# Kernel optimization log

Hardware: AMD Instinct MI355X
Metric: run time of the kernel (lower is better)

Reference implementation:

```python
import jax, jax.numpy as jnp
import numpy as np

N_NODES = 50000
N_EDGES = 800000
IN_CH = 3
HID = 32
OUT_CH = 16
HEADS = 8
NEG_SLOPE = 0.2  # PyG GATConv default LeakyReLU slope


def setup_inputs() -> dict:
    key = jax.random.key(0)
    ks = jax.random.split(key, 12)
    x = jax.random.normal(ks[0], (N_NODES, IN_CH), dtype=jnp.float32)
    edge_index = jax.random.randint(ks[1], (2, N_EDGES), 0, N_NODES, dtype=jnp.int64)
    # Layer 1: GATConv(3 -> 32, heads=8, concat=True)
    s1 = 1.0 / np.sqrt(IN_CH)
    W1 = jax.random.uniform(ks[2], (IN_CH, HEADS * HID), jnp.float32, -s1, s1)
    att_src1 = jax.random.uniform(ks[3], (HEADS, HID), jnp.float32, -s1, s1)
    att_dst1 = jax.random.uniform(ks[4], (HEADS, HID), jnp.float32, -s1, s1)
    bias1 = jnp.zeros((HEADS * HID,), jnp.float32)
    # Layer 2: GATConv(256 -> 16, heads=1, concat=False)
    s2 = 1.0 / np.sqrt(HEADS * HID)
    W2 = jax.random.uniform(ks[5], (HEADS * HID, 1 * OUT_CH), jnp.float32, -s2, s2)
    att_src2 = jax.random.uniform(ks[6], (1, OUT_CH), jnp.float32, -s2, s2)
    att_dst2 = jax.random.uniform(ks[7], (1, OUT_CH), jnp.float32, -s2, s2)
    bias2 = jnp.zeros((OUT_CH,), jnp.float32)
    return {"x": x, "edge_index": edge_index,
            "W1": W1, "att_src1": att_src1, "att_dst1": att_dst1, "bias1": bias1,
            "W2": W2, "att_src2": att_src2, "att_dst2": att_dst2, "bias2": bias2}


def gat_conv(x, src, dst, W, att_src, att_dst, bias, heads, out_ch, concat):
    """PyG-style GATConv (eval mode: attention dropout is identity).
    src/dst already include self-loops. Returns [N, heads*out_ch] or [N, out_ch]."""
    N = x.shape[0]
    h = (x @ W).reshape(N, heads, out_ch)                      # [N,H,C]
    a_s = jnp.einsum("nhc,hc->nh", h, att_src)                 # [N,H]
    a_d = jnp.einsum("nhc,hc->nh", h, att_dst)                 # [N,H]
    e = jax.nn.leaky_relu(a_s[src] + a_d[dst], NEG_SLOPE)      # [E,H]
    # segment softmax over incoming edges of each dst node
    m = jax.ops.segment_max(e, dst, num_segments=N)            # [N,H]
    e = jnp.exp(e - m[dst])
    denom = jax.ops.segment_sum(e, dst, num_segments=N)        # [N,H]
    alpha = e / (denom[dst] + 1e-16)                           # [E,H]
    msg = h[src] * alpha[:, :, None]                           # [E,H,C]
    out = jax.ops.segment_sum(msg, dst, num_segments=N)        # [N,H,C]
    out = out.reshape(N, heads * out_ch) if concat else out.mean(axis=1)
    return out + bias


def reference(x, edge_index, W1, att_src1, att_dst1, bias1, W2, att_src2, att_dst2, bias2):
    N = x.shape[0]
    loop = jnp.arange(N, dtype=edge_index.dtype)
    src = jnp.concatenate([edge_index[0], loop])  # add self-loops (PyG default)
    dst = jnp.concatenate([edge_index[1], loop])
    h = gat_conv(x, src, dst, W1, att_src1, att_dst1, bias1, HEADS, HID, True)
    h = jax.nn.elu(h)
    out = gat_conv(h, src, dst, W2, att_src2, att_dst2, bias2, 1, OUT_CH, False)
    return out
```

## Files before the change

kernel.cpp:

```cpp
#include <hip/hip_runtime.h>
#include <math.h>

#define N_NODES 50000
#define N_EDGES 800000
#define E_TOT   850000
#define HEADS   8
#define HID     32
#define C1      256
#define OUTC    16
#define NEG     0.2f
#define NB1     ((N_NODES + 255) / 256)

__device__ __forceinline__ float lrelu(float v) { return v > 0.0f ? v : NEG * v; }

__global__ __launch_bounds__(256) void k_setup(
    const float* __restrict__ x, const int* __restrict__ ei,
    const float* __restrict__ W1,
    const float* __restrict__ att_s1, const float* __restrict__ att_d1,
    const float* __restrict__ W2,
    const float* __restrict__ att_s2, const float* __restrict__ att_d2,
    float4* __restrict__ xp, int* __restrict__ cnt, int* __restrict__ rank,
    float* __restrict__ As1, float* __restrict__ Ad1,
    float* __restrict__ As2, float* __restrict__ Ad2)
{
    int t = threadIdx.x;
    int e = blockIdx.x * 256 + t;
    if (blockIdx.x == 0) {
        if (t < 24) {
            int k = t / 8, h = t % 8;
            float as = 0.0f, ad = 0.0f;
            for (int c = 0; c < HID; c++) {
                float w = W1[k * C1 + h * HID + c];
                as = fmaf(w, att_s1[h * HID + c], as);
                ad = fmaf(w, att_d1[h * HID + c], ad);
            }
            As1[k * 8 + h] = as; Ad1[k * 8 + h] = ad;
        }
        float as2 = 0.0f, ad2 = 0.0f;
        for (int j = 0; j < OUTC; j++) {
            float w = W2[t * OUTC + j];
            as2 = fmaf(w, att_s2[j], as2);
            ad2 = fmaf(w, att_d2[j], ad2);
        }
        As2[t] = as2; Ad2[t] = ad2;
    }
    if (e < N_NODES)
        xp[e] = make_float4(x[e * 3], x[e * 3 + 1], x[e * 3 + 2], 1.0f);
    if (e < E_TOT) {
        int d = (e < N_EDGES) ? ei[N_EDGES + e] : (e - N_EDGES);
        rank[e] = atomicAdd(&cnt[d], 1);
    }
}

__global__ void k_scan1(const int* __restrict__ cnt, int* __restrict__ part,
                        int* __restrict__ bsum)
{
    __shared__ int s[256];
    int tid = threadIdx.x;
    int i = blockIdx.x * 256 + tid;
    int v = (i < N_NODES) ? cnt[i] : 0;
    s[tid] = v;
    __syncthreads();
    for (int o = 1; o < 256; o <<= 1) {
        int t = (tid >= o) ? s[tid - o] : 0;
        __syncthreads();
        s[tid] += t;
        __syncthreads();
    }
    if (i < N_NODES) part[i] = s[tid] - v;
    if (tid == 255) bsum[blockIdx.x] = s[255];
}

__global__ void k_scan2(int* __restrict__ bsum)
{
    __shared__ int s[256];
    int tid = threadIdx.x;
    int v = (tid < NB1) ? bsum[tid] : 0;
    s[tid] = v;
    __syncthreads();
    for (int o = 1; o < 256; o <<= 1) {
        int t = (tid >= o) ? s[tid - o] : 0;
        __syncthreads();
        s[tid] += t;
        __syncthreads();
    }
    if (tid < NB1) bsum[tid] = s[tid] - v;
}

__global__ void k_scan3(const int* __restrict__ part, const int* __restrict__ bsum,
                        int* __restrict__ off)
{
    int i = blockIdx.x * 256 + threadIdx.x;
    if (i < N_NODES) off[i] = part[i] + bsum[blockIdx.x];
    if (i == 0) off[N_NODES] = E_TOT;
}

__global__ void k_fill(const int* __restrict__ ei, const int* __restrict__ rank,
                       const int* __restrict__ off, int* __restrict__ csr_src)
{
    int e = blockIdx.x * blockDim.x + threadIdx.x;
    if (e >= E_TOT) return;
    int s, d;
    if (e < N_EDGES) { s = ei[e]; d = ei[N_EDGES + e]; } else { s = d = e - N_EDGES; }
    csr_src[off[d] + rank[e]] = s;
}

__global__ __launch_bounds__(256) void k_agg1(
    const int* __restrict__ off, const int* __restrict__ csr_src,
    const float4* __restrict__ xp,
    const float* __restrict__ As1, const float* __restrict__ Ad1,
    float4* __restrict__ xaccw)
{
    int tid = threadIdx.x;
    int h = tid & 7;
    int dst = blockIdx.x * 32 + (tid >> 3);
    if (dst >= N_NODES) return;
    float s0 = As1[h], s1 = As1[8 + h], s2 = As1[16 + h];
    float d0 = Ad1[h], d1 = Ad1[8 + h], d2 = Ad1[16 + h];
    float4 xd = xp[dst];
    float ad = xd.x * d0 + xd.y * d1 + xd.z * d2;
    int beg = off[dst], end = off[dst + 1];
    float a0 = 0.0f, a1 = 0.0f, a2 = 0.0f, a3 = 0.0f;
    int nfull = beg + ((end - beg) & ~7);
    for (int base = beg; base < nfull; base += 8) {
        int sm = csr_src[base + h];
        float4 xv = xp[sm];
        #pragma unroll
        for (int j = 0; j < 8; j++) {
            float vx = __shfl(xv.x, j, 8);
            float vy = __shfl(xv.y, j, 8);
            float vz = __shfl(xv.z, j, 8);
            float as = vx * s0 + vy * s1 + vz * s2;
            float p = __expf(lrelu(as + ad));
            a0 = fmaf(p, vx, a0);
            a1 = fmaf(p, vy, a1);
            a2 = fmaf(p, vz, a2);
            a3 += p;
        }
    }
    if (nfull < end) {
        int idx = nfull + h;
        int sm = (idx < end) ? csr_src[idx] : 0;
        float4 xv = xp[sm];
        int m = end - nfull;
        for (int j = 0; j < m; j++) {
            float vx = __shfl(xv.x, j, 8);
            float vy = __shfl(xv.y, j, 8);
            float vz = __shfl(xv.z, j, 8);
            float as = vx * s0 + vy * s1 + vz * s2;
            float p = __expf(lrelu(as + ad));
            a0 = fmaf(p, vx, a0);
            a1 = fmaf(p, vy, a1);
            a2 = fmaf(p, vz, a2);
            a3 += p;
        }
    }
    xaccw[dst * 8 + h] = make_float4(a0, a1, a2, a3);
}

__global__ __launch_bounds__(256) void k_fin1h2(
    const float4* __restrict__ xaccw, const float* __restrict__ W1,
    const float* __restrict__ b1, const float* __restrict__ W2,
    const float* __restrict__ As2, const float* __restrict__ Ad2,
    float* __restrict__ h2, float* __restrict__ a_s2, float* __restrict__ a_d2)
{
    __shared__ float sW1[3 * C1];
    __shared__ float sAux[3 * C1];
    __shared__ float sW2t[OUTC][260];
    __shared__ float sElu[16][260];
    int t = threadIdx.x;
    for (int i = t; i < 3 * C1; i += 256) sW1[i] = W1[i];
    sAux[t] = b1[t]; sAux[C1 + t] = As2[t]; sAux[2 * C1 + t] = Ad2[t];
    for (int i = t; i < C1 * OUTC; i += 256) {
        int k = i >> 4, j = i & 15;
        sW2t[j][k] = W2[i];
    }
    __syncthreads();
    int n = t >> 4, l = t & 15;
    int node = blockIdx.x * 16 + n;
    float as = 0.0f, ad = 0.0f;
    for (int i = 0; i < 16; i++) {
        int c = l + 16 * i;
        int h = c >> 5;
        float4 xa = xaccw[node * 8 + h];
        float z = (xa.x * sW1[c] + xa.y * sW1[C1 + c] + xa.z * sW1[2 * C1 + c])
                  / (xa.w + 1e-16f) + sAux[c];
        float e = z > 0.0f ? z : expm1f(z);
        sElu[n][c] = e;
        as = fmaf(e, sAux[C1 + c], as);
        ad = fmaf(e, sAux[2 * C1 + c], ad);
    }
    for (int o = 1; o < 16; o <<= 1) {
        as += __shfl_xor(as, o, 64);
        ad += __shfl_xor(ad, o, 64);
    }
    if (l == 0) { a_s2[node] = as; a_d2[node] = ad; }
    __syncthreads();
    const float4* e4 = (const float4*)&sElu[n][0];
    const float4* w4 = (const float4*)&sW2t[l][0];
    float acc = 0.0f;
    #pragma unroll 8
    for (int k = 0; k < 64; k++) {
        float4 a = e4[k], b = w4[k];
        acc = fmaf(a.x, b.x, fmaf(a.y, b.y, fmaf(a.z, b.z, fmaf(a.w, b.w, acc))));
    }
    h2[node * OUTC + l] = acc;
}

__global__ __launch_bounds__(256) void k_agg2(
    const int* __restrict__ off, const int* __restrict__ csr_src,
    const float* __restrict__ a_s, const float* __restrict__ a_d,
    const float* __restrict__ h2, const float* __restrict__ bias,
    float* __restrict__ out)
{
    int tid = threadIdx.x;
    int c = tid & 15;
    int dst = blockIdx.x * 16 + (tid >> 4);
    if (dst >= N_NODES) return;
    int beg = off[dst], end = off[dst + 1];
    float ad = a_d[dst];
    float acc = 0.0f, denp = 0.0f;
    int nfull = beg + ((end - beg) & ~15);
    for (int base = beg; base < nfull; base += 16) {
        int sm = csr_src[base + c];
        float p = __expf(lrelu(a_s[sm] + ad));
        denp += p;
        #pragma unroll
        for (int j = 0; j < 16; j++) {
            int s = __shfl(sm, j, 16);
            float pj = __shfl(p, j, 16);
            acc = fmaf(pj, h2[s * OUTC + c], acc);
        }
    }
    if (nfull < end) {
        int idx = nfull + c;
        int sm = 0; float p = 0.0f;
        if (idx < end) { sm = csr_src[idx]; p = __expf(lrelu(a_s[sm] + ad)); }
        denp += p;
        int m = end - nfull;
        for (int j = 0; j < m; j++) {
            int s = __shfl(sm, j, 16);
            float pj = __shfl(p, j, 16);
            acc = fmaf(pj, h2[s * OUTC + c], acc);
        }
    }
    for (int o = 1; o < 16; o <<= 1) denp += __shfl_xor(denp, o, 16);
    out[dst * OUTC + c] = acc / (denp + 1e-16f) + bias[c];
}

extern "C" void kernel_launch(void* const* d_in, const int* in_sizes, int n_in,
                              void* d_out, int out_size, void* d_ws, size_t ws_size,
                              hipStream_t stream)
{
    (void)in_sizes; (void)n_in; (void)out_size; (void)ws_size;
    const float* x    = (const float*)d_in[0];
    const int*   ei   = (const int*)d_in[1];
    const float* W1   = (const float*)d_in[2];
    const float* as1w = (const float*)d_in[3];
    const float* ad1w = (const float*)d_in[4];
    const float* b1   = (const float*)d_in[5];
    const float* W2   = (const float*)d_in[6];
    const float* as2w = (const float*)d_in[7];
    const float* ad2w = (const float*)d_in[8];
    const float* b2   = (const float*)d_in[9];
    float* out = (float*)d_out;

    const long N = N_NODES;
    char* p = (char*)d_ws;
    auto alloc = [&](size_t elems) {
        void* r = p; p += ((elems + 3) & ~(size_t)3) * 4; return r;
    };

    float4* xp      = (float4*)alloc(N * 4);
    float4* xaccw   = (float4*)alloc(N * HEADS * 4);
    int*   cnt      = (int*)alloc(N);
    int*   part     = (int*)alloc(N);
    int*   off      = (int*)alloc(N + 1);
    int*   bsum     = (int*)alloc(256);
    int*   rank     = (int*)alloc(E_TOT);
    int*   csr_src  = (int*)alloc(E_TOT);
    float* As1      = (float*)alloc(32);
    float* Ad1      = (float*)alloc(32);
    float* As2      = (float*)alloc(C1);
    float* Ad2      = (float*)alloc(C1);
    float* h2v      = (float*)alloc(N * OUTC);
    float* a_s2     = (float*)alloc(N);
    float* a_d2     = (float*)alloc(N);

    hipMemsetAsync(cnt, 0, (size_t)N * sizeof(int), stream);

    k_setup<<<(E_TOT + 255) / 256, 256, 0, stream>>>(
        x, ei, W1, as1w, ad1w, W2, as2w, ad2w,
        xp, cnt, rank, As1, Ad1, As2, Ad2);
    k_scan1<<<NB1, 256, 0, stream>>>(cnt, part, bsum);
    k_scan2<<<1, 256, 0, stream>>>(bsum);
    k_scan3<<<NB1, 256, 0, stream>>>(part, bsum, off);
    k_fill<<<(E_TOT + 255) / 256, 256, 0, stream>>>(ei, rank, off, csr_src);

    k_agg1<<<(int)((N + 31) / 32), 256, 0, stream>>>(off, csr_src, xp, As1, Ad1, xaccw);
    k_fin1h2<<<(int)(N / 16), 256, 0, stream>>>(xaccw, W1, b1, W2, As2, Ad2, h2v, a_s2, a_d2);
    k_agg2<<<(int)((N + 15) / 16), 256, 0, stream>>>(off, csr_src, a_s2, a_d2, h2v, b2, out);
}
```

Before: 196.6 us.

## Fuse scans into single-pass kernel and merge layer-1 aggregation with finalize

Replaces the three scan kernels with one kernel that uses a last-block-done counter and a spin-wait flag to propagate block prefixes. Fuses the layer-1 edge aggregation into the finalize/h2 kernel, keeping per-node accumulators in shared memory instead of writing them to a global buffer. Each block recomputes the attention projections locally rather than in the setup kernel. The aim is fewer launches and less global traffic. The risks are that the spin-wait depends on all scan blocks being co-resident, and that the fused kernel has lower occupancy.

Result: slower. 239.3 us (+21.7%).

```diff
diff --git a/kernel.cpp b/kernel.cpp
--- a/kernel.cpp
+++ b/kernel.cpp
@@ -15,121 +15,143 @@
 
 __global__ __launch_bounds__(256) void k_setup(
     const float* __restrict__ x, const int* __restrict__ ei,
+    float4* __restrict__ xp, int* __restrict__ cnt, int* __restrict__ rank)
+{
+    int e = blockIdx.x * 256 + threadIdx.x;
+    if (e < N_NODES)
+        xp[e] = make_float4(x[e * 3], x[e * 3 + 1], x[e * 3 + 2], 1.0f);
+    if (e < E_TOT) {
+        int d = (e < N_EDGES) ? ei[N_EDGES + e] : (e - N_EDGES);
+        rank[e] = atomicAdd(&cnt[d], 1);
+    }
+}
+
+__global__ __launch_bounds__(256) void k_scanAll(
+    const int* __restrict__ cnt, int* __restrict__ off,
+    int* __restrict__ bsum, int* __restrict__ bpre, int* __restrict__ syncw)
+{
+    __shared__ int s[256];
+    __shared__ int sFlag;
+    int tid = threadIdx.x, bid = blockIdx.x;
+    int i = bid * 256 + tid;
+    int v = (i < N_NODES) ? cnt[i] : 0;
+    s[tid] = v;
+    __syncthreads();
+    for (int o = 1; o < 256; o <<= 1) {
+        int t2 = (tid >= o) ? s[tid - o] : 0;
+        __syncthreads();
+        s[tid] += t2;
+        __syncthreads();
+    }
+    int excl = s[tid] - v;
+    int total = s[255];
+    __syncthreads();
+    if (tid == 0) {
+        __hip_atomic_store(&bsum[bid], total, __ATOMIC_RELEASE, __HIP_MEMORY_SCOPE_AGENT);
+        int prev = __hip_atomic_fetch_add(&syncw[0], 1, __ATOMIC_ACQ_REL, __HIP_MEMORY_SCOPE_AGENT);
+        sFlag = (prev == NB1 - 1) ? 1 : 0;
+    }
+    __syncthreads();
+    if (sFlag) {
+        int bv = (tid < NB1) ? __hip_atomic_load(&bsum[tid], __ATOMIC_ACQUIRE, __HIP_MEMORY_SCOPE_AGENT) : 0;
+        s[tid] = bv;
+        __syncthreads();
+        for (int o = 1; o < 256; o <<= 1) {
+            int t2 = (tid >= o) ? s[tid - o] : 0;
+            __syncthreads();
+            s[tid] += t2;
+            __syncthreads();
+        }
+        if (tid < NB1)
+            __hip_atomic_store(&bpre[tid], s[tid] - bv, __ATOMIC_RELEASE, __HIP_MEMORY_SCOPE_AGENT);
+        __syncthreads();
+        if (tid == 0) {
+            __threadfence();
+            __hip_atomic_store(&syncw[1], 1, __ATOMIC_RELEASE, __HIP_MEMORY_SCOPE_AGENT);
+        }
+    }
+    if (tid == 0) {
+        while (__hip_atomic_load(&syncw[1], __ATOMIC_ACQUIRE, __HIP_MEMORY_SCOPE_AGENT) == 0)
+            __builtin_amdgcn_s_sleep(16);
+        sFlag = __hip_atomic_load(&bpre[bid], __ATOMIC_ACQUIRE, __HIP_MEMORY_SCOPE_AGENT);
+    }
+    __syncthreads();
+    int base = sFlag;
+    if (i < N_NODES) off[i] = base + excl;
+    if (i == 0) off[N_NODES] = E_TOT;
+}
+
+__global__ void k_fill(const int* __restrict__ ei, const int* __restrict__ rank,
+                       const int* __restrict__ off, int* __restrict__ csr_src)
+{
+    int e = blockIdx.x * blockDim.x + threadIdx.x;
+    if (e >= E_TOT) return;
+    int s, d;
+    if (e < N_EDGES) { s = ei[e]; d = ei[N_EDGES + e]; } else { s = d = e - N_EDGES; }
+    csr_src[off[d] + rank[e]] = s;
+}
+
+__global__ __launch_bounds__(256) void k_aggfin(
+    const int* __restrict__ off, const int* __restrict__ csr_src,
+    const float4* __restrict__ xp,
     const float* __restrict__ W1,
     const float* __restrict__ att_s1, const float* __restrict__ att_d1,
-    const float* __restrict__ W2,
+    const float* __restrict__ b1, const float* __restrict__ W2,
     const float* __restrict__ att_s2, const float* __restrict__ att_d2,
-    float4* __restrict__ xp, int* __restrict__ cnt, int* __restrict__ rank,
-    float* __restrict__ As1, float* __restrict__ Ad1,
-    float* __restrict__ As2, float* __restrict__ Ad2)
-{
+    float* __restrict__ h2, float* __restrict__ a_s2, float* __restrict__ a_d2)
+{
+    __shared__ float  sW1[3 * C1];
+    __shared__ float  sAux[3 * C1];
+    __shared__ float  sW2t[OUTC][272];
+    __shared__ float  sElu[16][272];
+    __shared__ float  sAtt[48];
+    __shared__ float4 sXac[16][8];
     int t = threadIdx.x;
-    int e = blockIdx.x * 256 + t;
-    if (blockIdx.x == 0) {
-        if (t < 24) {
-            int k = t / 8, h = t % 8;
-            float as = 0.0f, ad = 0.0f;
-            for (int c = 0; c < HID; c++) {
-                float w = W1[k * C1 + h * HID + c];
-                as = fmaf(w, att_s1[h * HID + c], as);
-                ad = fmaf(w, att_d1[h * HID + c], ad);
-            }
-            As1[k * 8 + h] = as; Ad1[k * 8 + h] = ad;
-        }
+    for (int i = t; i < 3 * C1; i += 256) sW1[i] = W1[i];
+    sAux[t] = b1[t];
+    {
         float as2 = 0.0f, ad2 = 0.0f;
         for (int j = 0; j < OUTC; j++) {
             float w = W2[t * OUTC + j];
             as2 = fmaf(w, att_s2[j], as2);
             ad2 = fmaf(w, att_d2[j], ad2);
         }
-        As2[t] = as2; Ad2[t] = ad2;
-    }
-    if (e < N_NODES)
-        xp[e] = make_float4(x[e * 3], x[e * 3 + 1], x[e * 3 + 2], 1.0f);
-    if (e < E_TOT) {
-        int d = (e < N_EDGES) ? ei[N_EDGES + e] : (e - N_EDGES);
-        rank[e] = atomicAdd(&cnt[d], 1);
-    }
-}
-
-__global__ void k_scan1(const int* __restrict__ cnt, int* __restrict__ part,
-                        int* __restrict__ bsum)
-{
-    __shared__ int s[256];
-    int tid = threadIdx.x;
-    int i = blockIdx.x * 256 + tid;
-    int v = (i < N_NODES) ? cnt[i] : 0;
-    s[tid] = v;
-    __syncthreads();
-    for (int o = 1; o < 256; o <<= 1) {
-        int t = (tid >= o) ? s[tid - o] : 0;
-        __syncthreads();
-        s[tid] += t;
-        __syncthreads();
-    }
-    if (i < N_NODES) part[i] = s[tid] - v;
-    if (tid == 255) bsum[blockIdx.x] = s[255];
-}
-
-__global__ void k_scan2(int* __restrict__ bsum)
-{
-    __shared__ int s[256];
-    int tid = threadIdx.x;
-    int v = (tid < NB1) ? bsum[tid] : 0;
-    s[tid] = v;
-    __syncthreads();
-    for (int o = 1; o < 256; o <<= 1) {
-        int t = (tid >= o) ? s[tid - o] : 0;
-        __syncthreads();
-        s[tid] += t;
-        __syncthreads();
-    }
-    if (tid < NB1) bsum[tid] = s[tid] - v;
-}
-
-__global__ void k_scan3(const int* __restrict__ part, const int* __restrict__ bsum,
-                        int* __restrict__ off)
-{
-    int i = blockIdx.x * 256 + threadIdx.x;
-    if (i < N_NODES) off[i] = part[i] + bsum[blockIdx.x];
-    if (i == 0) off[N_NODES] = E_TOT;
-}
-
-__global__ void k_fill(const int* __restrict__ ei, const int* __restrict__ rank,
-                       const int* __restrict__ off, int* __restrict__ csr_src)
-{
-    int e = blockIdx.x * blockDim.x + threadIdx.x;
-    if (e >= E_TOT) return;
-    int s, d;
-    if (e < N_EDGES) { s = ei[e]; d = ei[N_EDGES + e]; } else { s = d = e - N_EDGES; }
-    csr_src[off[d] + rank[e]] = s;
-}
-
-__global__ __launch_bounds__(256) void k_agg1(
-    const int* __restrict__ off, const int* __restrict__ csr_src,
-    const float4* __restrict__ xp,
-    const float* __restrict__ As1, const float* __restrict__ Ad1,
-    float4* __restrict__ xaccw)
-{
-    int tid = threadIdx.x;
-    int h = tid & 7;
-    int dst = blockIdx.x * 32 + (tid >> 3);
-    if (dst >= N_NODES) return;
-    float s0 = As1[h], s1 = As1[8 + h], s2 = As1[16 + h];
-    float d0 = Ad1[h], d1 = Ad1[8 + h], d2 = Ad1[16 + h];
-    float4 xd = xp[dst];
+        sAux[C1 + t] = as2; sAux[2 * C1 + t] = ad2;
+    }
+    for (int i = t; i < C1 * OUTC; i += 256) {
+        int k = i >> 4, j = i & 15;
+        sW2t[j][k] = W2[i];
+    }
+    if (t < 48) {
+        int q = t & 7, k = (t >> 3) % 3;
+        bool isD = t >= 24;
+        const float* att = isD ? att_d1 : att_s1;
+        float a = 0.0f;
+        for (int c = 0; c < HID; c++)
+            a = fmaf(W1[k * C1 + q * HID + c], att[q * HID + c], a);
+        sAtt[(isD ? 24 : 0) + k * 8 + q] = a;
+    }
+    __syncthreads();
+
+    int n = t >> 4, l = t & 15;
+    int h = l & 7, sub = l >> 3;
+    int node = blockIdx.x * 16 + n;
+    float s0 = sAtt[h],      s1 = sAtt[8 + h],  s2 = sAtt[16 + h];
+    float d0 = sAtt[24 + h], d1 = sAtt[32 + h], d2 = sAtt[40 + h];
+    float4 xd = xp[node];
     float ad = xd.x * d0 + xd.y * d1 + xd.z * d2;
-    int beg = off[dst], end = off[dst + 1];
+    int beg = off[node], end = off[node + 1];
     float a0 = 0.0f, a1 = 0.0f, a2 = 0.0f, a3 = 0.0f;
-    int nfull = beg + ((end - beg) & ~7);
-    for (int base = beg; base < nfull; base += 8) {
-        int sm = csr_src[base + h];
+    int nfull = beg + ((end - beg) & ~15);
+    for (int base = beg; base < nfull; base += 16) {
+        int sm = csr_src[base + l];
         float4 xv = xp[sm];
         #pragma unroll
         for (int j = 0; j < 8; j++) {
-            float vx = __shfl(xv.x, j, 8);
-            float vy = __shfl(xv.y, j, 8);
-            float vz = __shfl(xv.z, j, 8);
+            int jj = sub * 8 + j;
+            float vx = __shfl(xv.x, jj, 16);
+            float vy = __shfl(xv.y, jj, 16);
+            float vz = __shfl(xv.z, jj, 16);
             float as = vx * s0 + vy * s1 + vz * s2;
             float p = __expf(lrelu(as + ad));
             a0 = fmaf(p, vx, a0);
@@ -138,15 +160,15 @@
             a3 += p;
         }
     }
-    if (nfull < end) {
-        int idx = nfull + h;
-        int sm = (idx < end) ? csr_src[idx] : 0;
+    int m = end - nfull;
+    if (m > 0) {
+        int sm = csr_src[(l < m) ? (nfull + l) : nfull];
         float4 xv = xp[sm];
-        int m = end - nfull;
-        for (int j = 0; j < m; j++) {
-            float vx = __shfl(xv.x, j, 8);
-            float vy = __shfl(xv.y, j, 8);
-            float vz = __shfl(xv.z, j, 8);
+        int jbeg = sub * 8, jlim = min(jbeg + 8, m);
+        for (int j = jbeg; j < jlim; j++) {
+            float vx = __shfl(xv.x, j, 16);
+            float vy = __shfl(xv.y, j, 16);
+            float vz = __shfl(xv.z, j, 16);
             float as = vx * s0 + vy * s1 + vz * s2;
             float p = __expf(lrelu(as + ad));
             a0 = fmaf(p, vx, a0);
@@ -155,47 +177,32 @@
             a3 += p;
         }
     }
-    xaccw[dst * 8 + h] = make_float4(a0, a1, a2, a3);
-}
-
-__global__ __launch_bounds__(256) void k_fin1h2(
-    const float4* __restrict__ xaccw, const float* __restrict__ W1,
-    const float* __restrict__ b1, const float* __restrict__ W2,
-    const float* __restrict__ As2, const float* __restrict__ Ad2,
-    float* __restrict__ h2, float* __restrict__ a_s2, float* __restrict__ a_d2)
-{
-    __shared__ float sW1[3 * C1];
-    __shared__ float sAux[3 * C1];
-    __shared__ float sW2t[OUTC][260];
-    __shared__ float sElu[16][260];
-    int t = threadIdx.x;
-    for (int i = t; i < 3 * C1; i += 256) sW1[i] = W1[i];
-    sAux[t] = b1[t]; sAux[C1 + t] = As2[t]; sAux[2 * C1 + t] = Ad2[t];
-    for (int i = t; i < C1 * OUTC; i += 256) {
-        int k = i >> 4, j = i & 15;
-        sW2t[j][k] = W2[i];
-    }
-    __syncthreads();
-    int n = t >> 4, l = t & 15;
-    int node = blockIdx.x * 16 + n;
-    float as = 0.0f, ad = 0.0f;
+    a0 += __shfl_xor(a0, 8, 16);
+    a1 += __shfl_xor(a1, 8, 16);
+    a2 += __shfl_xor(a2, 8, 16);
+    a3 += __shfl_xor(a3, 8, 16);
+    if (sub == 0) sXac[n][h] = make_float4(a0, a1, a2, a3);
+    __syncthreads();
+
+    float as2v = 0.0f, ad2v = 0.0f;
     for (int i = 0; i < 16; i++) {
         int c = l + 16 * i;
-        int h = c >> 5;
-        float4 xa = xaccw[node * 8 + h];
+        int hh = c >> 5;
+        float4 xa = sXac[n][hh];
         float z = (xa.x * sW1[c] + xa.y * sW1[C1 + c] + xa.z * sW1[2 * C1 + c])
                   / (xa.w + 1e-16f) + sAux[c];
         float e = z > 0.0f ? z : expm1f(z);
         sElu[n][c] = e;
-        as = fmaf(e, sAux[C1 + c], as);
-        ad = fmaf(e, sAux[2 * C1 + c], ad);
+        as2v = fmaf(e, sAux[C1 + c], as2v);
+        ad2v = fmaf(e, sAux[2 * C1 + c], ad2v);
     }
     for (int o = 1; o < 16; o <<= 1) {
-        as += __shfl_xor(as, o, 64);
-        ad += __shfl_xor(ad, o, 64);
-    }
-    if (l == 0) { a_s2[node] = as; a_d2[node] = ad; }
-    __syncthreads();
+        as2v += __shfl_xor(as2v, o, 16);
+        ad2v += __shfl_xor(ad2v, o, 16);
+    }
+    if (l == 0) { a_s2[node] = as2v; a_d2[node] = ad2v; }
+    __syncthreads();
+
     const float4* e4 = (const float4*)&sElu[n][0];
     const float4* w4 = (const float4*)&sW2t[l][0];
     float acc = 0.0f;
@@ -237,8 +244,8 @@
         int sm = 0; float p = 0.0f;
         if (idx < end) { sm = csr_src[idx]; p = __expf(lrelu(a_s[sm] + ad)); }
         denp += p;
-        int m = end - nfull;
-        for (int j = 0; j < m; j++) {
+        int mm = end - nfull;
+        for (int j = 0; j < mm; j++) {
             int s = __shfl(sm, j, 16);
             float pj = __shfl(p, j, 16);
             acc = fmaf(pj, h2[s * OUTC + c], acc);
@@ -272,32 +279,23 @@
     };
 
     float4* xp      = (float4*)alloc(N * 4);
-    float4* xaccw   = (float4*)alloc(N * HEADS * 4);
-    int*   cnt      = (int*)alloc(N);
-    int*   part     = (int*)alloc(N);
+    int*   cnt      = (int*)alloc(N + 8);
+    int*   syncw    = cnt + N;
+    int*   bsum     = (int*)alloc(256);
+    int*   bpre     = (int*)alloc(256);
     int*   off      = (int*)alloc(N + 1);
-    int*   bsum     = (int*)alloc(256);
     int*   rank     = (int*)alloc(E_TOT);
     int*   csr_src  = (int*)alloc(E_TOT);
-    float* As1      = (float*)alloc(32);
-    float* Ad1      = (float*)alloc(32);
-    float* As2      = (float*)alloc(C1);
-    float* Ad2      = (float*)alloc(C1);
     float* h2v      = (float*)alloc(N * OUTC);
     float* a_s2     = (float*)alloc(N);
     float* a_d2     = (float*)alloc(N);
 
-    hipMemsetAsync(cnt, 0, (size_t)N * sizeof(int), stream);
-
-    k_setup<<<(E_TOT + 255) / 256, 256, 0, stream>>>(
-        x, ei, W1, as1w, ad1w, W2, as2w, ad2w,
-        xp, cnt, rank, As1, Ad1, As2, Ad2);
-    k_scan1<<<NB1, 256, 0, stream>>>(cnt, part, bsum);
-    k_scan2<<<1, 256, 0, stream>>>(bsum);
-    k_scan3<<<NB1, 256, 0, stream>>>(part, bsum, off);
+    hipMemsetAsync(cnt, 0, (size_t)(N + 2) * sizeof(int), stream);
+
+    k_setup<<<(E_TOT + 255) / 256, 256, 0, stream>>>(x, ei, xp, cnt, rank);
+    k_scanAll<<<NB1, 256, 0, stream>>>(cnt, off, bsum, bpre, syncw);
     k_fill<<<(E_TOT + 255) / 256, 256, 0, stream>>>(ei, rank, off, csr_src);
-
-    k_agg1<<<(int)((N + 31) / 32), 256, 0, stream>>>(off, csr_src, xp, As1, Ad1, xaccw);
-    k_fin1h2<<<(int)(N / 16), 256, 0, stream>>>(xaccw, W1, b1, W2, As2, Ad2, h2v, a_s2, a_d2);
-    k_agg2<<<(int)((N + 15) / 16), 256, 0, stream>>>(off, csr_src, a_s2, a_d2, h2v, b2, out);
-}
+    k_aggfin<<<(int)(N / 16), 256, 0, stream>>>(
+        off, csr_src, xp, W1, as1w, ad1w, b1, W2, as2w, ad2w, h2v, a_s2, a_d2);
+    k_agg2<<<(int)(N / 16), 256, 0, stream>>>(off, csr_src, a_s2, a_d2, h2v, b2, out);
+}
```

## Merge scan passes, software-prefetch edge chunks, and widen agg1 to 16 lanes per node

Applied to the files above, without the earlier changes.

The scan2 and scan3 kernels are merged into one: each block reduces the preceding block sums itself, which removes a launch. The attention-weight precomputation moves out of k_setup into per-block recomputation inside agg1 and fin1h2. Both aggregation kernels now prefetch the next 16-edge chunk's source index and features while the current chunk is processed. agg1 now uses 16 lanes per node, two half-groups of 8 that each handle half the edges, combined with a shuffle at the end. The price is redundant small recomputation in every block and a larger per-block serial reduction of block sums.

Measured after the change: 199.4 us. About the same (+1.5%).

```diff
diff --git a/kernel.cpp b/kernel.cpp
--- a/kernel.cpp
+++ b/kernel.cpp
@@ -15,35 +15,9 @@
 
 __global__ __launch_bounds__(256) void k_setup(
     const float* __restrict__ x, const int* __restrict__ ei,
-    const float* __restrict__ W1,
-    const float* __restrict__ att_s1, const float* __restrict__ att_d1,
-    const float* __restrict__ W2,
-    const float* __restrict__ att_s2, const float* __restrict__ att_d2,
-    float4* __restrict__ xp, int* __restrict__ cnt, int* __restrict__ rank,
-    float* __restrict__ As1, float* __restrict__ Ad1,
-    float* __restrict__ As2, float* __restrict__ Ad2)
-{
-    int t = threadIdx.x;
-    int e = blockIdx.x * 256 + t;
-    if (blockIdx.x == 0) {
-        if (t < 24) {
-            int k = t / 8, h = t % 8;
-            float as = 0.0f, ad = 0.0f;
-            for (int c = 0; c < HID; c++) {
-                float w = W1[k * C1 + h * HID + c];
-                as = fmaf(w, att_s1[h * HID + c], as);
-                ad = fmaf(w, att_d1[h * HID + c], ad);
-            }
-            As1[k * 8 + h] = as; Ad1[k * 8 + h] = ad;
-        }
-        float as2 = 0.0f, ad2 = 0.0f;
-        for (int j = 0; j < OUTC; j++) {
-            float w = W2[t * OUTC + j];
-            as2 = fmaf(w, att_s2[j], as2);
-            ad2 = fmaf(w, att_d2[j], ad2);
-        }
-        As2[t] = as2; Ad2[t] = ad2;
-    }
+    float4* __restrict__ xp, int* __restrict__ cnt, int* __restrict__ rank)
+{
+    int e = blockIdx.x * 256 + threadIdx.x;
     if (e < N_NODES)
         xp[e] = make_float4(x[e * 3], x[e * 3 + 1], x[e * 3 + 2], 1.0f);
     if (e < E_TOT) {
@@ -71,27 +45,22 @@
     if (tid == 255) bsum[blockIdx.x] = s[255];
 }
 
-__global__ void k_scan2(int* __restrict__ bsum)
-{
-    __shared__ int s[256];
-    int tid = threadIdx.x;
-    int v = (tid < NB1) ? bsum[tid] : 0;
-    s[tid] = v;
-    __syncthreads();
-    for (int o = 1; o < 256; o <<= 1) {
-        int t = (tid >= o) ? s[tid - o] : 0;
+__global__ void k_scan23(const int* __restrict__ part, const int* __restrict__ bsum,
+                         int* __restrict__ off)
+{
+    __shared__ int sred[256];
+    int tid = threadIdx.x, bid = blockIdx.x;
+    int acc = 0;
+    for (int t = tid; t < bid; t += 256) acc += bsum[t];
+    sred[tid] = acc;
+    __syncthreads();
+    for (int o = 128; o > 0; o >>= 1) {
+        if (tid < o) sred[tid] += sred[tid + o];
         __syncthreads();
-        s[tid] += t;
-        __syncthreads();
-    }
-    if (tid < NB1) bsum[tid] = s[tid] - v;
-}
-
-__global__ void k_scan3(const int* __restrict__ part, const int* __restrict__ bsum,
-                        int* __restrict__ off)
-{
-    int i = blockIdx.x * 256 + threadIdx.x;
-    if (i < N_NODES) off[i] = part[i] + bsum[blockIdx.x];
+    }
+    int base = sred[0];
+    int i = bid * 256 + tid;
+    if (i < N_NODES) off[i] = part[i] + base;
     if (i == 0) off[N_NODES] = E_TOT;
 }
 
@@ -108,28 +77,50 @@
 __global__ __launch_bounds__(256) void k_agg1(
     const int* __restrict__ off, const int* __restrict__ csr_src,
     const float4* __restrict__ xp,
-    const float* __restrict__ As1, const float* __restrict__ Ad1,
+    const float* __restrict__ W1,
+    const float* __restrict__ att_s1, const float* __restrict__ att_d1,
     float4* __restrict__ xaccw)
 {
+    __shared__ float sAtt[48];
     int tid = threadIdx.x;
-    int h = tid & 7;
-    int dst = blockIdx.x * 32 + (tid >> 3);
-    if (dst >= N_NODES) return;
-    float s0 = As1[h], s1 = As1[8 + h], s2 = As1[16 + h];
-    float d0 = Ad1[h], d1 = Ad1[8 + h], d2 = Ad1[16 + h];
+    if (tid < 48) {
+        int q = tid & 7, k = (tid >> 3) % 3;
+        bool isD = tid >= 24;
+        const float* att = isD ? att_d1 : att_s1;
+        float a = 0.0f;
+        for (int c = 0; c < HID; c++)
+            a = fmaf(W1[k * C1 + q * HID + c], att[q * HID + c], a);
+        sAtt[(isD ? 24 : 0) + k * 8 + q] = a;
+    }
+    __syncthreads();
+    int l = tid & 15, h = l & 7, sub = l >> 3;
+    int dst = blockIdx.x * 16 + (tid >> 4);
+    float s0 = sAtt[h],      s1 = sAtt[8 + h],  s2 = sAtt[16 + h];
+    float d0 = sAtt[24 + h], d1 = sAtt[32 + h], d2 = sAtt[40 + h];
     float4 xd = xp[dst];
     float ad = xd.x * d0 + xd.y * d1 + xd.z * d2;
     int beg = off[dst], end = off[dst + 1];
     float a0 = 0.0f, a1 = 0.0f, a2 = 0.0f, a3 = 0.0f;
-    int nfull = beg + ((end - beg) & ~7);
-    for (int base = beg; base < nfull; base += 8) {
-        int sm = csr_src[base + h];
-        float4 xv = xp[sm];
-        #pragma unroll
-        for (int j = 0; j < 8; j++) {
-            float vx = __shfl(xv.x, j, 8);
-            float vy = __shfl(xv.y, j, 8);
-            float vz = __shfl(xv.z, j, 8);
+    int nb = (end - beg + 15) >> 4;
+    int idx = beg + l;
+    int sm = csr_src[(idx < end) ? idx : beg];
+    float4 xv = xp[sm];
+    for (int b = 0; b < nb; b++) {
+        int base = beg + (b << 4);
+        float4 xc = xv;
+        if (b + 1 < nb) {
+            int nidx = base + 16 + l;
+            sm = csr_src[(nidx < end) ? nidx : (base + 16)];
+            xv = xp[sm];
+        }
+        int rem = end - base;
+        int mlim = rem < 16 ? rem : 16;
+        int jbeg = sub * 8;
+        int jlim = jbeg + 8 < mlim ? jbeg + 8 : mlim;
+        for (int j = jbeg; j < jlim; j++) {
+            float vx = __shfl(xc.x, j, 16);
+            float vy = __shfl(xc.y, j, 16);
+            float vz = __shfl(xc.z, j, 16);
             float as = vx * s0 + vy * s1 + vz * s2;
             float p = __expf(lrelu(as + ad));
             a0 = fmaf(p, vx, a0);
@@ -138,30 +129,17 @@
             a3 += p;
         }
     }
-    if (nfull < end) {
-        int idx = nfull + h;
-        int sm = (idx < end) ? csr_src[idx] : 0;
-        float4 xv = xp[sm];
-        int m = end - nfull;
-        for (int j = 0; j < m; j++) {
-            float vx = __shfl(xv.x, j, 8);
-            float vy = __shfl(xv.y, j, 8);
-            float vz = __shfl(xv.z, j, 8);
-            float as = vx * s0 + vy * s1 + vz * s2;
-            float p = __expf(lrelu(as + ad));
-            a0 = fmaf(p, vx, a0);
-            a1 = fmaf(p, vy, a1);
-            a2 = fmaf(p, vz, a2);
-            a3 += p;
-        }
-    }
-    xaccw[dst * 8 + h] = make_float4(a0, a1, a2, a3);
+    a0 += __shfl_xor(a0, 8, 16);
+    a1 += __shfl_xor(a1, 8, 16);
+    a2 += __shfl_xor(a2, 8, 16);
+    a3 += __shfl_xor(a3, 8, 16);
+    if (sub == 0) xaccw[dst * 8 + h] = make_float4(a0, a1, a2, a3);
 }
 
 __global__ __launch_bounds__(256) void k_fin1h2(
     const float4* __restrict__ xaccw, const float* __restrict__ W1,
     const float* __restrict__ b1, const float* __restrict__ W2,
-    const float* __restrict__ As2, const float* __restrict__ Ad2,
+    const float* __restrict__ att_s2, const float* __restrict__ att_d2,
     float* __restrict__ h2, float* __restrict__ a_s2, float* __restrict__ a_d2)
 {
     __shared__ float sW1[3 * C1];
@@ -170,7 +148,16 @@
     __shared__ float sElu[16][260];
     int t = threadIdx.x;
     for (int i = t; i < 3 * C1; i += 256) sW1[i] = W1[i];
-    sAux[t] = b1[t]; sAux[C1 + t] = As2[t]; sAux[2 * C1 + t] = Ad2[t];
+    sAux[t] = b1[t];
+    {
+        float as2 = 0.0f, ad2 = 0.0f;
+        for (int j = 0; j < OUTC; j++) {
+            float w = W2[t * OUTC + j];
+            as2 = fmaf(w, att_s2[j], as2);
+            ad2 = fmaf(w, att_d2[j], ad2);
+        }
+        sAux[C1 + t] = as2; sAux[2 * C1 + t] = ad2;
+    }
     for (int i = t; i < C1 * OUTC; i += 256) {
         int k = i >> 4, j = i & 15;
         sW2t[j][k] = W2[i];
@@ -216,32 +203,39 @@
     int tid = threadIdx.x;
     int c = tid & 15;
     int dst = blockIdx.x * 16 + (tid >> 4);
-    if (dst >= N_NODES) return;
     int beg = off[dst], end = off[dst + 1];
     float ad = a_d[dst];
     float acc = 0.0f, denp = 0.0f;
-    int nfull = beg + ((end - beg) & ~15);
-    for (int base = beg; base < nfull; base += 16) {
-        int sm = csr_src[base + c];
-        float p = __expf(lrelu(a_s[sm] + ad));
+    int nb = (end - beg + 15) >> 4;
+    int idx = beg + c;
+    int sm = csr_src[(idx < end) ? idx : beg];
+    float asv = a_s[sm];
+    for (int b = 0; b < nb; b++) {
+        int base = beg + (b << 4);
+        int smc = sm; float asc = asv;
+        bool valid = (base + c) < end;
+        if (b + 1 < nb) {
+            int nidx = base + 16 + c;
+            sm = csr_src[(nidx < end) ? nidx : (base + 16)];
+            asv = a_s[sm];
+        }
+        float p = valid ? __expf(lrelu(asc + ad)) : 0.0f;
         denp += p;
-        #pragma unroll
-        for (int j = 0; j < 16; j++) {
-            int s = __shfl(sm, j, 16);
-            float pj = __shfl(p, j, 16);
-            acc = fmaf(pj, h2[s * OUTC + c], acc);
-        }
-    }
-    if (nfull < end) {
-        int idx = nfull + c;
-        int sm = 0; float p = 0.0f;
-        if (idx < end) { sm = csr_src[idx]; p = __expf(lrelu(a_s[sm] + ad)); }
-        denp += p;
-        int m = end - nfull;
-        for (int j = 0; j < m; j++) {
-            int s = __shfl(sm, j, 16);
-            float pj = __shfl(p, j, 16);
-            acc = fmaf(pj, h2[s * OUTC + c], acc);
+        int rem = end - base;
+        int mlim = rem < 16 ? rem : 16;
+        if (mlim == 16) {
+            #pragma unroll
+            for (int j = 0; j < 16; j++) {
+                int s = __shfl(smc, j, 16);
+                float pj = __shfl(p, j, 16);
+                acc = fmaf(pj, h2[s * OUTC + c], acc);
+            }
+        } else {
+            for (int j = 0; j < mlim; j++) {
+                int s = __shfl(smc, j, 16);
+                float pj = __shfl(p, j, 16);
+                acc = fmaf(pj, h2[s * OUTC + c], acc);
+            }
         }
     }
     for (int o = 1; o < 16; o <<= 1) denp += __shfl_xor(denp, o, 16);
@@ -279,25 +273,18 @@
     int*   bsum     = (int*)alloc(256);
     int*   rank     = (int*)alloc(E_TOT);
     int*   csr_src  = (int*)alloc(E_TOT);
-    float* As1      = (float*)alloc(32);
-    float* Ad1      = (float*)alloc(32);
-    float* As2      = (float*)alloc(C1);
-    float* Ad2      = (float*)alloc(C1);
     float* h2v      = (float*)alloc(N * OUTC);
     float* a_s2     = (float*)alloc(N);
     float* a_d2     = (float*)alloc(N);
 
     hipMemsetAsync(cnt, 0, (size_t)N * sizeof(int), stream);
 
-    k_setup<<<(E_TOT + 255) / 256, 256, 0, stream>>>(
-        x, ei, W1, as1w, ad1w, W2, as2w, ad2w,
-        xp, cnt, rank, As1, Ad1, As2, Ad2);
+    k_setup<<<(E_TOT + 255) / 256, 256, 0, stream>>>(x, ei, xp, cnt, rank);
     k_scan1<<<NB1, 256, 0, stream>>>(cnt, part, bsum);
-    k_scan2<<<1, 256, 0, stream>>>(bsum);
-    k_scan3<<<NB1, 256, 0, stream>>>(part, bsum, off);
+    k_scan23<<<NB1, 256, 0, stream>>>(part, bsum, off);
     k_fill<<<(E_TOT + 255) / 256, 256, 0, stream>>>(ei, rank, off, csr_src);
 
-    k_agg1<<<(int)((N + 31) / 32), 256, 0, stream>>>(off, csr_src, xp, As1, Ad1, xaccw);
-    k_fin1h2<<<(int)(N / 16), 256, 0, stream>>>(xaccw, W1, b1, W2, As2, Ad2, h2v, a_s2, a_d2);
-    k_agg2<<<(int)((N + 15) / 16), 256, 0, stream>>>(off, csr_src, a_s2, a_d2, h2v, b2, out);
-}
+    k_agg1<<<(int)(N / 16), 256, 0, stream>>>(off, csr_src, xp, W1, as1w, ad1w, xaccw);
+    k_fin1h2<<<(int)(N / 16), 256, 0, stream>>>(xaccw, W1, b1, W2, as2w, ad2w, h2v, a_s2, a_d2);
+    k_agg2<<<(int)(N / 16), 256, 0, stream>>>(off, csr_src, a_s2, a_d2, h2v, b2, out);
+}
```
